# Kernel tuning notes

Measured on AMD Instinct MI355X. Metric: run time of the kernel, lower is better.

Reference implementation:

```python
import jax, jax.numpy as jnp
import numpy as np

B, H, W, C = 32, 56, 56, 384
WS, SS, NH = 7, 3, 12
HD = C // NH
SCALE = HD ** -0.5
N = WS * WS
NW = (H // WS) * (W // WS)
HIDDEN = 4 * C
EPS = 1e-5


def _rel_pos_index():
    coords = np.stack(np.meshgrid(np.arange(WS), np.arange(WS), indexing='ij')).reshape(2, -1)
    rel = coords[:, :, None] - coords[:, None, :]
    rel = rel.transpose(1, 2, 0).astype(np.int64)
    rel[..., 0] += WS - 1
    rel[..., 1] += WS - 1
    rel[..., 0] *= 2 * WS - 1
    return rel.sum(-1)  # [N, N]


def _attn_mask():
    img = np.zeros((H, W), dtype=np.float32)
    slices = (slice(0, -WS), slice(-WS, -SS), slice(-SS, None))
    cnt = 0
    for hs in slices:
        for ws_ in slices:
            img[hs, ws_] = cnt
            cnt += 1
    mw = img.reshape(H // WS, WS, W // WS, WS).transpose(0, 2, 1, 3).reshape(-1, N)  # [nW, N]
    am = mw[:, None, :] - mw[:, :, None]
    return np.where(am != 0, -100.0, 0.0).astype(np.float32)  # [nW, N, N]


REL_IDX = jnp.asarray(_rel_pos_index())
ATTN_MASK = jnp.asarray(_attn_mask())


def _ln(x, g, b):
    mu = x.mean(-1, keepdims=True)
    var = ((x - mu) ** 2).mean(-1, keepdims=True)
    return (x - mu) * jax.lax.rsqrt(var + EPS) * g + b


def setup_inputs() -> dict:
    key = jax.random.key(0)
    ks = jax.random.split(key, 16)
    s = 0.02
    return {
        'x': jax.random.normal(ks[0], (B, H * W, C), jnp.float32),
        'norm1_g': jnp.ones((C,), jnp.float32),
        'norm1_b': jnp.zeros((C,), jnp.float32),
        'qkv_w': jax.random.normal(ks[1], (C, 3 * C), jnp.float32) * s,
        'qkv_b': jnp.zeros((3 * C,), jnp.float32),
        'bias_table': jax.random.normal(ks[2], ((2 * WS - 1) ** 2, NH), jnp.float32) * s,
        'proj_w': jax.random.normal(ks[3], (C, C), jnp.float32) * s,
        'proj_b': jnp.zeros((C,), jnp.float32),
        'norm2_g': jnp.ones((C,), jnp.float32),
        'norm2_b': jnp.zeros((C,), jnp.float32),
        'fc1_w': jax.random.normal(ks[4], (C, HIDDEN), jnp.float32) * s,
        'fc1_b': jnp.zeros((HIDDEN,), jnp.float32),
        'fc2_w': jax.random.normal(ks[5], (HIDDEN, C), jnp.float32) * s,
        'fc2_b': jnp.zeros((C,), jnp.float32),
    }


def reference(x, norm1_g, norm1_b, qkv_w, qkv_b, bias_table, proj_w, proj_b,
              norm2_g, norm2_b, fc1_w, fc1_b, fc2_w, fc2_b):
    shortcut = x
    h = _ln(x, norm1_g, norm1_b).reshape(B, H, W, C)
    # cyclic shift
    h = jnp.roll(h, shift=(-SS, -SS), axis=(1, 2))
    # window partition -> [B*nW, N, C]
    hw = h.reshape(B, H // WS, WS, W // WS, WS, C).transpose(0, 1, 3, 2, 4, 5).reshape(-1, N, C)
    Bw = hw.shape[0]
    # qkv
    qkv = (hw @ qkv_w + qkv_b).reshape(Bw, N, 3, NH, HD).transpose(2, 0, 3, 1, 4)
    q, k, v = qkv[0] * SCALE, qkv[1], qkv[2]  # [Bw, NH, N, HD]
    attn = jnp.einsum('whnd,whmd->whnm', q, k)
    rel_bias = bias_table[REL_IDX.reshape(-1)].reshape(N, N, NH).transpose(2, 0, 1)
    attn = attn + rel_bias[None]
    # shift mask: [Bw] = [B, nW]
    attn = attn.reshape(B, NW, NH, N, N) + ATTN_MASK[None, :, None]
    attn = jax.nn.softmax(attn.reshape(Bw, NH, N, N), axis=-1)
    o = jnp.einsum('whnm,whmd->whnd', attn, v).transpose(0, 2, 1, 3).reshape(Bw, N, C)
    o = o @ proj_w + proj_b
    # window reverse + reverse shift
    o = o.reshape(B, H // WS, W // WS, WS, WS, C).transpose(0, 1, 3, 2, 4, 5).reshape(B, H, W, C)
    o = jnp.roll(o, shift=(SS, SS), axis=(1, 2)).reshape(B, H * W, C)
    x = shortcut + o
    # MLP
    m = _ln(x, norm2_g, norm2_b)
    m = jax.nn.gelu(m @ fc1_w + fc1_b, approximate=False)
    m = m @ fc2_w + fc2_b
    return x + m
```

## Files before the change

kernel.cpp:

```cpp
#include <hip/hip_runtime.h>
#include <hip/hip_bf16.h>
#include <cstdint>
#include <cstddef>

static constexpr int Bv  = 32;
static constexpr int Cv  = 384;
static constexpr int Nv  = 49;
static constexpr int Mv  = 32 * 64 * 49;
static constexpr float SCALEv = 0.17677669529663687f;

using bf16 = __hip_bfloat16;
typedef __bf16 bf16x8 __attribute__((ext_vector_type(8)));
typedef float  f32x4  __attribute__((ext_vector_type(4)));

__global__ __launch_bounds__(256)
void wt_kernel(const float* __restrict__ w, bf16* __restrict__ wt, int K, int N) {
    int idx = blockIdx.x * 256 + threadIdx.x;
    if (idx >= K * N) return;
    int n = idx / K, k = idx - n * K;
    wt[idx] = (bf16)w[(size_t)k * N + n];
}

__global__ __launch_bounds__(256)
void bm_kernel(const float* __restrict__ btab, float* __restrict__ bmt) {
    const int cls = blockIdx.x, h = blockIdx.y;
    for (int idx = threadIdx.x; idx < 4096; idx += 256) {
        int col = idx >> 6, row = idx & 63;
        float v;
        if (col >= 49) {
            v = -1e30f;
        } else {
            int n = row < 49 ? row : 48;
            int m = col;
            int i1 = n / 7, j1 = n - i1 * 7;
            int i2 = m / 7, j2 = m - i2 * 7;
            v = btab[((i1 - i2 + 6) * 13 + (j1 - j2 + 6)) * 12 + h];
            int lh1 = (cls & 2) ? (i1 < 4 ? 1 : 2) : 0;
            int lw1 = (cls & 1) ? (j1 < 4 ? 1 : 2) : 0;
            int lh2 = (cls & 2) ? (i2 < 4 ? 1 : 2) : 0;
            int lw2 = (cls & 1) ? (j2 < 4 ? 1 : 2) : 0;
            if ((lh1 * 3 + lw1) != (lh2 * 3 + lw2)) v += -100.f;
        }
        bmt[((size_t)(cls * 12 + h) * 64 + col) * 64 + row] = v;
    }
}

template <int MODE>
__global__ __launch_bounds__(256)
void ln_kernel(const float* __restrict__ src, const float* __restrict__ gam,
               const float* __restrict__ bet, bf16* __restrict__ dst) {
    const int wave = threadIdx.x >> 6, lane = threadIdx.x & 63;
    const int r = blockIdx.x * 4 + wave;
    size_t srow;
    if (MODE == 0) {
        int w  = r / 49, n = r - w * 49;
        int b  = w >> 6, win = w & 63;
        int hb = win >> 3, wb = win & 7;
        int ii = n / 7, jj = n - ii * 7;
        int hh = hb * 7 + ii + 3; if (hh >= 56) hh -= 56;
        int ww = wb * 7 + jj + 3; if (ww >= 56) ww -= 56;
        srow = (size_t)b * 3136 + hh * 56 + ww;
    } else {
        srow = (size_t)r;
    }
    const float* p = src + srow * 384;
    float vals[6];
    float s = 0.f, s2 = 0.f;
#pragma unroll
    for (int t = 0; t < 6; ++t) {
        float v = p[t * 64 + lane];
        vals[t] = v; s += v; s2 += v * v;
    }
#pragma unroll
    for (int o = 32; o > 0; o >>= 1) {
        s  += __shfl_xor(s,  o, 64);
        s2 += __shfl_xor(s2, o, 64);
    }
    const float mu  = s * (1.f / 384.f);
    const float var = s2 * (1.f / 384.f) - mu * mu;
    const float rs  = rsqrtf(var + 1e-5f);
    bf16* q = dst + (size_t)r * 384;
#pragma unroll
    for (int t = 0; t < 6; ++t) {
        int e = t * 64 + lane;
        q[e] = (bf16)((vals[t] - mu) * rs * gam[e] + bet[e]);
    }
}

__global__ __launch_bounds__(64)
void attn_kernel(const bf16* __restrict__ qkv, const float* __restrict__ bmt,
                 bf16* __restrict__ o) {
    const int w = blockIdx.x;
    const int h = blockIdx.y;
    const int lane = threadIdx.x;
    const int quad = lane >> 4, l16 = lane & 15;
    __shared__ bf16 Vt[32][72];
    __shared__ bf16 Ps[64][72];

    const size_t rowbase = (size_t)w * 49;

    for (int idx = lane; idx < 49 * 16; idx += 64) {
        int row = idx >> 4, dp = (idx & 15) << 1;
        const bf16* src = qkv + (rowbase + row) * 1152 + 768 + h * 32 + dp;
        Vt[dp][row]     = src[0];
        Vt[dp + 1][row] = src[1];
    }
    for (int idx = lane; idx < 512; idx += 64) {
        int d = idx >> 4, c = idx & 15;
        if (c) Vt[d][48 + c] = (bf16)0.f;
    }

    f32x4 acc[4][4] = {};
    bf16x8 af[4], bfr[4];
#pragma unroll
    for (int i = 0; i < 4; ++i) {
        int row = 16 * i + l16; if (row > 48) row = 48;
        af[i] = *(const bf16x8*)(qkv + (rowbase + row) * 1152 + h * 32 + quad * 8);
    }
#pragma unroll
    for (int j = 0; j < 4; ++j) {
        int row = 16 * j + l16; if (row > 48) row = 48;
        bfr[j] = *(const bf16x8*)(qkv + (rowbase + row) * 1152 + 384 + h * 32 + quad * 8);
    }
#pragma unroll
    for (int i = 0; i < 4; ++i)
#pragma unroll
        for (int j = 0; j < 4; ++j)
            acc[i][j] = __builtin_amdgcn_mfma_f32_16x16x32_bf16(af[i], bfr[j], acc[i][j], 0, 0, 0);

    const int cls = (((w & 63) >= 56) ? 2 : 0) + (((w & 7) == 7) ? 1 : 0);
    const float* bmbase = bmt + (size_t)(cls * 12 + h) * 4096;
    float inv[4][4];
#pragma unroll
    for (int i = 0; i < 4; ++i) {
        f32x4 bm[4];
#pragma unroll
        for (int j = 0; j < 4; ++j)
            bm[j] = *(const f32x4*)(bmbase + (16 * j + l16) * 64 + 16 * i + quad * 4);
#pragma unroll
        for (int t = 0; t < 4; ++t) {
            float v0 = acc[i][0][t] + bm[0][t];
            float v1 = acc[i][1][t] + bm[1][t];
            float v2 = acc[i][2][t] + bm[2][t];
            float v3 = acc[i][3][t] + bm[3][t];
            float mx = fmaxf(fmaxf(v0, v1), fmaxf(v2, v3));
#pragma unroll
            for (int ofs = 1; ofs < 16; ofs <<= 1) mx = fmaxf(mx, __shfl_xor(mx, ofs, 64));
            float p0 = __expf(v0 - mx), p1 = __expf(v1 - mx);
            float p2 = __expf(v2 - mx), p3 = __expf(v3 - mx);
            float s = (p0 + p1) + (p2 + p3);
#pragma unroll
            for (int ofs = 1; ofs < 16; ofs <<= 1) s += __shfl_xor(s, ofs, 64);
            inv[i][t] = 1.f / s;
            int prow = 16 * i + quad * 4 + t;
            Ps[prow][l16]      = (bf16)p0;
            Ps[prow][16 + l16] = (bf16)p1;
            Ps[prow][32 + l16] = (bf16)p2;
            Ps[prow][48 + l16] = (bf16)p3;
        }
    }
    __syncthreads();

    f32x4 oacc[4][2] = {};
    bf16x8 vb[2][2];
#pragma unroll
    for (int jn = 0; jn < 2; ++jn)
#pragma unroll
        for (int ks = 0; ks < 2; ++ks)
            vb[jn][ks] = *(const bf16x8*)(&Vt[16 * jn + l16][32 * ks + quad * 8]);
#pragma unroll
    for (int i = 0; i < 4; ++i) {
#pragma unroll
        for (int ks = 0; ks < 2; ++ks) {
            bf16x8 pa = *(const bf16x8*)(&Ps[16 * i + l16][32 * ks + quad * 8]);
#pragma unroll
            for (int jn = 0; jn < 2; ++jn)
                oacc[i][jn] = __builtin_amdgcn_mfma_f32_16x16x32_bf16(pa, vb[jn][ks], oacc[i][jn], 0, 0, 0);
        }
    }

#pragma unroll
    for (int i = 0; i < 4; ++i) {
        int nbase = 16 * i + quad * 4;
#pragma unroll
        for (int t = 0; t < 4; ++t) {
            int n = nbase + t;
            if (n < 49) {
                bf16* dst = o + (rowbase + n) * 384 + h * 32;
                dst[l16]      = (bf16)(oacc[i][0][t] * inv[i][t]);
                dst[16 + l16] = (bf16)(oacc[i][1][t] * inv[i][t]);
            }
        }
    }
}

template <int EPI>
__global__ __launch_bounds__(256)
void gemm_bt(const bf16* __restrict__ A, const bf16* __restrict__ Bt,
             const float* __restrict__ bias, int N, int K,
             bf16* __restrict__ outb, float* __restrict__ outf,
             const float* __restrict__ resid) {
    __shared__ bf16 As[128 * 64];
    __shared__ bf16 Bs[128 * 64];
    const int tid  = threadIdx.x;
    const int lane = tid & 63, wave = tid >> 6;
    const int quad = lane >> 4, l16 = lane & 15;
    const int wm = wave >> 1, wn = wave & 1;
    const long m0 = (long)blockIdx.y * 128;
    const long n0 = (long)blockIdx.x * 128;

    f32x4 acc[4][4] = {};

    for (int k0 = 0; k0 < K; k0 += 64) {
        __syncthreads();
#pragma unroll
        for (int it = 0; it < 4; ++it) {
            int e = it * 256 + tid;
            int row = e >> 3;
            int col = (e & 7) << 3;
            __builtin_amdgcn_global_load_lds(
                (const __attribute__((address_space(1))) unsigned int*)(A + (size_t)(m0 + row) * K + k0 + col),
                (__attribute__((address_space(3))) unsigned int*)(As + (size_t)e * 8),
                16, 0, 0);
            __builtin_amdgcn_global_load_lds(
                (const __attribute__((address_space(1))) unsigned int*)(Bt + (size_t)(n0 + row) * K + k0 + col),
                (__attribute__((address_space(3))) unsigned int*)(Bs + (size_t)e * 8),
                16, 0, 0);
        }
        __syncthreads();
#pragma unroll
        for (int kk = 0; kk < 64; kk += 32) {
            bf16x8 af[4], bfr[4];
#pragma unroll
            for (int i = 0; i < 4; ++i)
                af[i] = *(const bf16x8*)(As + (wm * 64 + i * 16 + l16) * 64 + kk + quad * 8);
#pragma unroll
            for (int j = 0; j < 4; ++j)
                bfr[j] = *(const bf16x8*)(Bs + (wn * 64 + j * 16 + l16) * 64 + kk + quad * 8);
#pragma unroll
            for (int i = 0; i < 4; ++i)
#pragma unroll
                for (int j = 0; j < 4; ++j)
                    acc[i][j] = __builtin_amdgcn_mfma_f32_16x16x32_bf16(af[i], bfr[j], acc[i][j], 0, 0, 0);
        }
    }

#pragma unroll
    for (int i = 0; i < 4; ++i) {
        const long mbase = m0 + wm * 64 + i * 16 + quad * 4;
#pragma unroll
        for (int j = 0; j < 4; ++j) {
            const int col = (int)n0 + wn * 64 + j * 16 + l16;
            const float bv = bias[col];
            f32x4 r = acc[i][j];
#pragma unroll
            for (int t = 0; t < 4; ++t) {
                const long m = mbase + t;
                float val = r[t] + bv;
                if constexpr (EPI == 0) {
                    float sc = (col < 384) ? SCALEv : 1.0f;
                    outb[(size_t)m * N + col] = (bf16)(val * sc);
                } else if constexpr (EPI == 1) {
                    int w  = (int)(m / 49), n = (int)(m - (long)w * 49);
                    int b  = w >> 6, win = w & 63;
                    int hb = win >> 3, wb = win & 7;
                    int ii = n / 7, jj = n - ii * 7;
                    int hh = hb * 7 + ii + 3; if (hh >= 56) hh -= 56;
                    int ww = wb * 7 + jj + 3; if (ww >= 56) ww -= 56;
                    size_t dst = ((size_t)b * 3136 + hh * 56 + ww) * 384 + col;
                    outf[dst] = resid[dst] + val;
                } else if constexpr (EPI == 2) {
                    float g = 0.5f * val * (1.0f + erff(val * 0.70710678118654752f));
                    outb[(size_t)m * N + col] = (bf16)g;
                } else {
                    size_t oo = (size_t)m * N + col;
                    outf[oo] = resid[oo] + val;
                }
            }
        }
    }
}

extern "C" void kernel_launch(void* const* d_in, const int* in_sizes, int n_in,
                              void* d_out, int out_size, void* d_ws, size_t ws_size,
                              hipStream_t stream) {
    const float* x     = (const float*)d_in[0];
    const float* n1g   = (const float*)d_in[1];
    const float* n1b   = (const float*)d_in[2];
    const float* qkvw  = (const float*)d_in[3];
    const float* qkvb  = (const float*)d_in[4];
    const float* btab  = (const float*)d_in[5];
    const float* projw = (const float*)d_in[6];
    const float* projb = (const float*)d_in[7];
    const float* n2g   = (const float*)d_in[8];
    const float* n2b   = (const float*)d_in[9];
    const float* fc1w  = (const float*)d_in[10];
    const float* fc1b  = (const float*)d_in[11];
    const float* fc2w  = (const float*)d_in[12];
    const float* fc2b  = (const float*)d_in[13];
    float* out = (float*)d_out;

    char* ws = (char*)d_ws;
    size_t off = 0;
    auto take = [&](size_t bytes) {
        char* p = ws + off;
        off += (bytes + 255) & ~(size_t)255;
        return p;
    };
    bf16* qkv_wt  = (bf16*)take((size_t)1152 * 384 * 2);
    bf16* proj_wt = (bf16*)take((size_t)384 * 384 * 2);
    bf16* fc1_wt  = (bf16*)take((size_t)1536 * 384 * 2);
    bf16* fc2_wt  = (bf16*)take((size_t)384 * 1536 * 2);
    float* bmt    = (float*)take((size_t)4 * 12 * 64 * 64 * 4);
    bf16* qkv_buf = (bf16*)take((size_t)Mv * 1152 * 2);
    bf16* o_buf   = (bf16*)take((size_t)Mv * 384 * 2);
    bf16* hw_buf  = (bf16*)take((size_t)Mv * 384 * 2);
    float* x1     = (float*)take((size_t)Mv * 384 * 4);
    bf16* g_buf   = qkv_buf;
    bf16* x1n     = hw_buf;

    wt_kernel<<<(384 * 1152 + 255) / 256, 256, 0, stream>>>(qkvw,  qkv_wt,  384, 1152);
    wt_kernel<<<(384 * 384  + 255) / 256, 256, 0, stream>>>(projw, proj_wt, 384, 384);
    wt_kernel<<<(384 * 1536 + 255) / 256, 256, 0, stream>>>(fc1w,  fc1_wt,  384, 1536);
    wt_kernel<<<(1536 * 384 + 255) / 256, 256, 0, stream>>>(fc2w,  fc2_wt,  1536, 384);
    bm_kernel<<<dim3(4, 12), 256, 0, stream>>>(btab, bmt);
    ln_kernel<0><<<Mv / 4, 256, 0, stream>>>(x, n1g, n1b, hw_buf);
    gemm_bt<0><<<dim3(1152 / 128, Mv / 128), 256, 0, stream>>>(
        hw_buf, qkv_wt, qkvb, 1152, 384, qkv_buf, nullptr, nullptr);
    attn_kernel<<<dim3(2048, 12), 64, 0, stream>>>(qkv_buf, bmt, o_buf);
    gemm_bt<1><<<dim3(384 / 128, Mv / 128), 256, 0, stream>>>(
        o_buf, proj_wt, projb, 384, 384, nullptr, x1, x);
    ln_kernel<1><<<Mv / 4, 256, 0, stream>>>(x1, n2g, n2b, x1n);
    gemm_bt<2><<<dim3(1536 / 128, Mv / 128), 256, 0, stream>>>(
        x1n, fc1_wt, fc1b, 1536, 384, g_buf, nullptr, nullptr);
    gemm_bt<3><<<dim3(384 / 128, Mv / 128), 256, 0, stream>>>(
        g_buf, fc2_wt, fc2b, 384, 1536, nullptr, out, x1);
}
```

Before: 1.326 ms.

## Fuse LayerNorm2, fc1+GELU and fc2+residual into one MLP kernel

Replaces the LN2 kernel and the two MLP GEMMs with a single kernel. Each 64-row block normalizes its rows into LDS, then computes the hidden layer in 128-column chunks, applies GELU into LDS and accumulates fc2 in registers, finishing with the residual add. This removes the round trip of the normalized activations and the large GELU intermediate through global memory, plus two launches. In exchange the weights are read directly from global memory with no LDS tiling, rows per block are fewer (64 instead of 128 tiles) and register pressure is high.

Measured after the change: 1.349 ms. No clear change (+1.8%).

```diff
diff --git a/kernel.cpp b/kernel.cpp
--- a/kernel.cpp
+++ b/kernel.cpp
@@ -3,9 +3,6 @@
 #include <cstdint>
 #include <cstddef>
 
-static constexpr int Bv  = 32;
-static constexpr int Cv  = 384;
-static constexpr int Nv  = 49;
 static constexpr int Mv  = 32 * 64 * 49;
 static constexpr float SCALEv = 0.17677669529663687f;
 
@@ -45,24 +42,18 @@
     }
 }
 
-template <int MODE>
 __global__ __launch_bounds__(256)
 void ln_kernel(const float* __restrict__ src, const float* __restrict__ gam,
                const float* __restrict__ bet, bf16* __restrict__ dst) {
     const int wave = threadIdx.x >> 6, lane = threadIdx.x & 63;
     const int r = blockIdx.x * 4 + wave;
-    size_t srow;
-    if (MODE == 0) {
-        int w  = r / 49, n = r - w * 49;
-        int b  = w >> 6, win = w & 63;
-        int hb = win >> 3, wb = win & 7;
-        int ii = n / 7, jj = n - ii * 7;
-        int hh = hb * 7 + ii + 3; if (hh >= 56) hh -= 56;
-        int ww = wb * 7 + jj + 3; if (ww >= 56) ww -= 56;
-        srow = (size_t)b * 3136 + hh * 56 + ww;
-    } else {
-        srow = (size_t)r;
-    }
+    int w  = r / 49, n = r - w * 49;
+    int b  = w >> 6, win = w & 63;
+    int hb = win >> 3, wb = win & 7;
+    int ii = n / 7, jj = n - ii * 7;
+    int hh = hb * 7 + ii + 3; if (hh >= 56) hh -= 56;
+    int ww = wb * 7 + jj + 3; if (ww >= 56) ww -= 56;
+    size_t srow = (size_t)b * 3136 + hh * 56 + ww;
     const float* p = src + srow * 384;
     float vals[6];
     float s = 0.f, s2 = 0.f;
@@ -260,7 +251,7 @@
                 if constexpr (EPI == 0) {
                     float sc = (col < 384) ? SCALEv : 1.0f;
                     outb[(size_t)m * N + col] = (bf16)(val * sc);
-                } else if constexpr (EPI == 1) {
+                } else {
                     int w  = (int)(m / 49), n = (int)(m - (long)w * 49);
                     int b  = w >> 6, win = w & 63;
                     int hb = win >> 3, wb = win & 7;
@@ -269,13 +260,119 @@
                     int ww = wb * 7 + jj + 3; if (ww >= 56) ww -= 56;
                     size_t dst = ((size_t)b * 3136 + hh * 56 + ww) * 384 + col;
                     outf[dst] = resid[dst] + val;
-                } else if constexpr (EPI == 2) {
-                    float g = 0.5f * val * (1.0f + erff(val * 0.70710678118654752f));
-                    outb[(size_t)m * N + col] = (bf16)g;
-                } else {
-                    size_t oo = (size_t)m * N + col;
-                    outf[oo] = resid[oo] + val;
                 }
+            }
+        }
+    }
+}
+
+__global__ __launch_bounds__(256, 2)
+void mlp_kernel(const float* __restrict__ x1,
+                const float* __restrict__ gam, const float* __restrict__ bet,
+                const bf16* __restrict__ W1t, const float* __restrict__ b1,
+                const bf16* __restrict__ W2t, const float* __restrict__ b2,
+                float* __restrict__ out) {
+    constexpr int ASTR = 392;
+    constexpr int GSTR = 136;
+    __shared__ bf16 A_lds[64 * ASTR];
+    __shared__ bf16 G_lds[64 * GSTR];
+
+    const int tid  = threadIdx.x;
+    const int lane = tid & 63, wv = tid >> 6;
+    const int quad = lane >> 4, l16 = lane & 15;
+    const long r0 = (long)blockIdx.x * 64;
+
+    float g6[6], be6[6];
+#pragma unroll
+    for (int t = 0; t < 6; ++t) { g6[t] = gam[t * 64 + lane]; be6[t] = bet[t * 64 + lane]; }
+    for (int rr = 0; rr < 16; ++rr) {
+        const int row = wv * 16 + rr;
+        const float* p = x1 + (r0 + row) * 384;
+        float vals[6], s = 0.f, s2 = 0.f;
+#pragma unroll
+        for (int t = 0; t < 6; ++t) {
+            float v = p[t * 64 + lane];
+            vals[t] = v; s += v; s2 += v * v;
+        }
+#pragma unroll
+        for (int o = 32; o > 0; o >>= 1) {
+            s  += __shfl_xor(s,  o, 64);
+            s2 += __shfl_xor(s2, o, 64);
+        }
+        const float mu  = s * (1.f / 384.f);
+        const float var = s2 * (1.f / 384.f) - mu * mu;
+        const float rs  = rsqrtf(var + 1e-5f);
+#pragma unroll
+        for (int t = 0; t < 6; ++t)
+            A_lds[row * ASTR + t * 64 + lane] = (bf16)((vals[t] - mu) * rs * g6[t] + be6[t]);
+    }
+
+    f32x4 oacc[4][6] = {};
+    __syncthreads();
+
+    for (int hh = 0; hh < 12; ++hh) {
+        f32x4 acc1[4][2] = {};
+#pragma unroll
+        for (int k0 = 0; k0 < 384; k0 += 32) {
+            bf16x8 af[4], bf2[2];
+#pragma unroll
+            for (int i = 0; i < 4; ++i)
+                af[i] = *(const bf16x8*)(A_lds + (16 * i + l16) * ASTR + k0 + quad * 8);
+#pragma unroll
+            for (int j = 0; j < 2; ++j)
+                bf2[j] = *(const bf16x8*)(W1t + (size_t)(hh * 128 + wv * 32 + j * 16 + l16) * 384 + k0 + quad * 8);
+#pragma unroll
+            for (int i = 0; i < 4; ++i)
+#pragma unroll
+                for (int j = 0; j < 2; ++j)
+                    acc1[i][j] = __builtin_amdgcn_mfma_f32_16x16x32_bf16(af[i], bf2[j], acc1[i][j], 0, 0, 0);
+        }
+        __syncthreads();
+#pragma unroll
+        for (int j = 0; j < 2; ++j) {
+            const float bv = b1[hh * 128 + wv * 32 + j * 16 + l16];
+#pragma unroll
+            for (int i = 0; i < 4; ++i) {
+#pragma unroll
+                for (int t = 0; t < 4; ++t) {
+                    float v = acc1[i][j][t] + bv;
+                    float gl = 0.5f * v * (1.0f + erff(v * 0.70710678118654752f));
+                    G_lds[(16 * i + quad * 4 + t) * GSTR + wv * 32 + j * 16 + l16] = (bf16)gl;
+                }
+            }
+        }
+        __syncthreads();
+#pragma unroll
+        for (int k0 = 0; k0 < 128; k0 += 32) {
+            bf16x8 ga[4], wb[6];
+#pragma unroll
+            for (int i = 0; i < 4; ++i)
+                ga[i] = *(const bf16x8*)(G_lds + (16 * i + l16) * GSTR + k0 + quad * 8);
+#pragma unroll
+            for (int j = 0; j < 6; ++j)
+                wb[j] = *(const bf16x8*)(W2t + (size_t)(wv * 96 + j * 16 + l16) * 1536 + hh * 128 + k0 + quad * 8);
+#pragma unroll
+            for (int i = 0; i < 4; ++i)
+#pragma unroll
+                for (int j = 0; j < 6; ++j)
+                    oacc[i][j] = __builtin_amdgcn_mfma_f32_16x16x32_bf16(ga[i], wb[j], oacc[i][j], 0, 0, 0);
+        }
+    }
+
+    float bv[6];
+#pragma unroll
+    for (int j = 0; j < 6; ++j) bv[j] = b2[wv * 96 + j * 16 + l16];
+#pragma unroll
+    for (int i = 0; i < 4; ++i) {
+#pragma unroll
+        for (int t = 0; t < 4; ++t) {
+            const long r = r0 + 16 * i + quad * 4 + t;
+            const float* rp = x1 + r * 384;
+            float* op = out + r * 384;
+#pragma unroll
+            for (int j = 0; j < 6; ++j) {
+                int col = wv * 96 + j * 16 + l16;
+                op[col] = rp[col] + bv[j] + oacc[i][j][t];
             }
         }
     }
@@ -316,23 +413,18 @@
     bf16* o_buf   = (bf16*)take((size_t)Mv * 384 * 2);
     bf16* hw_buf  = (bf16*)take((size_t)Mv * 384 * 2);
     float* x1     = (float*)take((size_t)Mv * 384 * 4);
-    bf16* g_buf   = qkv_buf;
-    bf16* x1n     = hw_buf;
 
     wt_kernel<<<(384 * 1152 + 255) / 256, 256, 0, stream>>>(qkvw,  qkv_wt,  384, 1152);
     wt_kernel<<<(384 * 384  + 255) / 256, 256, 0, stream>>>(projw, proj_wt, 384, 384);
     wt_kernel<<<(384 * 1536 + 255) / 256, 256, 0, stream>>>(fc1w,  fc1_wt,  384, 1536);
     wt_kernel<<<(1536 * 384 + 255) / 256, 256, 0, stream>>>(fc2w,  fc2_wt,  1536, 384);
     bm_kernel<<<dim3(4, 12), 256, 0, stream>>>(btab, bmt);
-    ln_kernel<0><<<Mv / 4, 256, 0, stream>>>(x, n1g, n1b, hw_buf);
+    ln_kernel<<<Mv / 4, 256, 0, stream>>>(x, n1g, n1b, hw_buf);
     gemm_bt<0><<<dim3(1152 / 128, Mv / 128), 256, 0, stream>>>(
         hw_buf, qkv_wt, qkvb, 1152, 384, qkv_buf, nullptr, nullptr);
     attn_kernel<<<dim3(2048, 12), 64, 0, stream>>>(qkv_buf, bmt, o_buf);
     gemm_bt<1><<<dim3(384 / 128, Mv / 128), 256, 0, stream>>>(
         o_buf, proj_wt, projb, 384, 384, nullptr, x1, x);
-    ln_kernel<1><<<Mv / 4, 256, 0, stream>>>(x1, n2g, n2b, x1n);
-    gemm_bt<2><<<dim3(1536 / 128, Mv / 128), 256, 0, stream>>>(
-        x1n, fc1_wt, fc1b, 1536, 384, g_buf, nullptr, nullptr);
-    gemm_bt<3><<<dim3(384 / 128, Mv / 128), 256, 0, stream>>>(
-        g_buf, fc2_wt, fc2b, 384, 1536, nullptr, out, x1);
-}
+    mlp_kernel<<<Mv / 64, 256, 0, stream>>>(
+        x1, n2g, n2b, fc1_wt, fc1b, fc2_wt, fc2b, out);
+}
```
